# Kernel tuning notes

Measured on AMD Instinct MI355X. Metric: run time of the kernel, lower is better.

The kernel has to match this reference:

```python
import jax, jax.numpy as jnp
import numpy as np

N_NODES = 20000
IN_CH = 512
HEADS = 8
CH = 64  # hidden_layer per head
E = 320000
E_LABEL = 100000


def setup_inputs() -> dict:
    key = jax.random.key(0)
    ks = jax.random.split(key, 8)
    x = jax.random.normal(ks[0], (N_NODES, IN_CH), dtype=jnp.float32)
    edge_index = jax.random.randint(ks[1], (2, E), 0, N_NODES)
    edge_label_index = jax.random.randint(ks[2], (2, E_LABEL), 0, N_NODES)
    # GATv2Conv params (share_weights=False, bias=True)
    sc = 1.0 / np.sqrt(IN_CH)
    W_l = jax.random.normal(ks[3], (IN_CH, HEADS * CH), dtype=jnp.float32) * sc
    W_r = jax.random.normal(ks[4], (IN_CH, HEADS * CH), dtype=jnp.float32) * sc
    att = jax.random.normal(ks[5], (HEADS, CH), dtype=jnp.float32) * (1.0 / np.sqrt(CH))
    bias = jnp.zeros((HEADS * CH,), dtype=jnp.float32)
    gamma = jnp.ones((HEADS * CH,), dtype=jnp.float32)
    beta = jnp.zeros((HEADS * CH,), dtype=jnp.float32)
    return {"x": x, "edge_index": edge_index, "edge_label_index": edge_label_index,
            "W_l": W_l, "W_r": W_r, "att": att, "bias": bias,
            "gamma": gamma, "beta": beta}


def reference(x, edge_index, edge_label_index, W_l, W_r, att, bias, gamma, beta):
    N = x.shape[0]
    H, C = att.shape
    src, dst = edge_index[0], edge_index[1]
    # GATv2Conv: separate source/target linear maps
    xl = (x @ W_l).reshape(N, H, C)
    xr = (x @ W_r).reshape(N, H, C)
    # per-edge attention logits (GATv2: leaky_relu BEFORE attention vector)
    e = jax.nn.leaky_relu(xl[src] + xr[dst], negative_slope=0.2)  # [E,H,C]
    alpha = jnp.einsum('ehc,hc->eh', e, att)                      # [E,H]
    # softmax over incoming edges of each destination node
    amax = jax.ops.segment_max(alpha, dst, num_segments=N)        # [N,H]
    alpha = jnp.exp(alpha - amax[dst])
    denom = jax.ops.segment_sum(alpha, dst, num_segments=N)       # [N,H]
    alpha = alpha / (denom[dst] + 1e-16)
    # scatter-add aggregation of attended source messages
    out = jax.ops.segment_sum(alpha[:, :, None] * xl[src], dst, num_segments=N)  # [N,H,C]
    out = out.reshape(N, H * C) + bias
    # BatchNorm1d (training-mode batch stats, eps=1e-5)
    mu = out.mean(axis=0)
    var = out.var(axis=0)
    out = (out - mu) * jax.lax.rsqrt(var + 1e-5) * gamma + beta
    out = jax.nn.relu(out)  # dropout is identity in deterministic reference
    # gather + dot-product link scoring
    s = out[edge_label_index[0]]
    t = out[edge_label_index[1]]
    return jnp.sum(s * t, axis=1)  # [E_LABEL]
```

## Files before the change

### kernel.cpp

```cpp
#include <hip/hip_runtime.h>
#include <hip/hip_bf16.h>
#include <cstdint>

#define IN_CH 512
#define HC    512
#define HEADS 8
#define NPACK 1024

typedef __attribute__((ext_vector_type(8))) short bf16x8;
typedef __attribute__((ext_vector_type(8))) ushort u16x8;
typedef __attribute__((ext_vector_type(4))) float f32x4;
typedef const __attribute__((address_space(1))) uint8_t* gaddr_t;
typedef __attribute__((address_space(3))) uint8_t* laddr_t;

__device__ inline ushort f2bf(float f) {
  uint32_t u = __float_as_uint(f);
  return (ushort)((u + 0x7fffu + ((u >> 16) & 1u)) >> 16);
}
__device__ inline float bf2f(ushort u) {
  return __uint_as_float(((uint32_t)u) << 16);
}

__global__ void prep(const float* __restrict__ x, ushort* __restrict__ xb,
                     const float* __restrict__ Wl, const float* __restrict__ Wr,
                     ushort* __restrict__ bt,
                     const int* __restrict__ ei, int* __restrict__ counts,
                     const int* __restrict__ eli, int* __restrict__ counts2,
                     int n4, int E, int EL, int nbc, int nbp, int nbh) {
  const int b = blockIdx.x;
  if (b < nbc) {
    const int i = b * 256 + threadIdx.x;
    if (i < n4) {
      const float4 v = ((const float4*)x)[i];
      ushort4 o;
      o.x = f2bf(v.x); o.y = f2bf(v.y); o.z = f2bf(v.z); o.w = f2bf(v.w);
      ((ushort4*)xb)[i] = o;
    }
  } else if (b < nbc + nbp) {
    const int i = (b - nbc) * 256 + threadIdx.x;
    if (i < NPACK * IN_CH) {
      const int n = i >> 9, k = i & 511;
      const float v = (n < HC) ? Wl[(size_t)k * HC + n] : Wr[(size_t)k * HC + (n - HC)];
      bt[i] = f2bf(v);
    }
  } else if (b < nbc + nbp + nbh) {
    const int e = (b - nbc - nbp) * 256 + threadIdx.x;
    if (e < E) atomicAdd(&counts[ei[E + e]], 1);
  } else {
    const int e = (b - nbc - nbp - nbh) * 256 + threadIdx.x;
    if (e < EL) atomicAdd(&counts2[eli[e]], 1);
  }
}

__global__ __launch_bounds__(256) void gemm_mfma(
    const ushort* __restrict__ xb, const ushort* __restrict__ bt,
    ushort* __restrict__ xlb, ushort* __restrict__ xrb, int M) {
  __shared__ __align__(16) ushort As[128 * 32];
  __shared__ __align__(16) ushort Bs[128 * 32];
  const int wave = threadIdx.x >> 6, lane = threadIdx.x & 63;
  const int row0 = blockIdx.y * 128, col0 = blockIdx.x * 128;
  const int quad = lane >> 4, m16 = lane & 15;
  const int wrow = (wave >> 1) * 64, wcol = (wave & 1) * 64;
  const int srow = lane >> 2;
  const int scol = (lane & 3) * 8;
  const f32x4 zero = {0.f, 0.f, 0.f, 0.f};
  f32x4 acc[4][4];
  #pragma unroll
  for (int i = 0; i < 4; ++i)
    #pragma unroll
    for (int j = 0; j < 4; ++j) acc[i][j] = zero;

  for (int k0 = 0; k0 < IN_CH; k0 += 32) {
    #pragma unroll
    for (int c = 0; c < 2; ++c) {
      const int chunk = wave * 2 + c;
      const ushort* ga = xb + (size_t)(row0 + chunk * 16 + srow) * IN_CH + k0 + scol;
      __builtin_amdgcn_global_load_lds((gaddr_t)ga, (laddr_t)(As + chunk * 512), 16, 0, 0);
      const ushort* gb = bt + (size_t)(col0 + chunk * 16 + srow) * IN_CH + k0 + scol;
      __builtin_amdgcn_global_load_lds((gaddr_t)gb, (laddr_t)(Bs + chunk * 512), 16, 0, 0);
    }
    __syncthreads();
    bf16x8 af[4], bfr[4];
    #pragma unroll
    for (int i = 0; i < 4; ++i)
      af[i] = *(const bf16x8*)(As + (wrow + i * 16 + m16) * 32 + quad * 8);
    #pragma unroll
    for (int j = 0; j < 4; ++j)
      bfr[j] = *(const bf16x8*)(Bs + (wcol + j * 16 + m16) * 32 + quad * 8);
    #pragma unroll
    for (int i = 0; i < 4; ++i)
      #pragma unroll
      for (int j = 0; j < 4; ++j)
        acc[i][j] = __builtin_amdgcn_mfma_f32_16x16x32_bf16(af[i], bfr[j], acc[i][j], 0, 0, 0);
    __syncthreads();
  }
  const bool isL = (col0 < HC);
  ushort* dst = isL ? xlb : xrb;
  const int cbase = isL ? col0 : (col0 - HC);
  #pragma unroll
  for (int i = 0; i < 4; ++i) {
    const int r = row0 + wrow + i * 16 + quad * 4;
    #pragma unroll
    for (int j = 0; j < 4; ++j) {
      const int cg = cbase + wcol + j * 16 + m16;
      #pragma unroll
      for (int t = 0; t < 4; ++t) {
        const int rr = r + t;
        if (rr < M) dst[(size_t)rr * HC + cg] = f2bf(acc[i][j][t]);
      }
    }
  }
}

__global__ void scan1(const int* __restrict__ cA, int* __restrict__ oA, int* __restrict__ bA,
                      const int* __restrict__ cB, int* __restrict__ oB, int* __restrict__ bB,
                      int Nn, int nb) {
  const int half = (blockIdx.x >= nb) ? 1 : 0;
  const int blk  = blockIdx.x - half * nb;
  const int* counts = half ? cB : cA;
  int* offsets = half ? oB : oA;
  int* bsums   = half ? bB : bA;
  __shared__ int tmp[256];
  const int t = threadIdx.x;
  const int i = blk * 256 + t;
  const int v = (i < Nn) ? counts[i] : 0;
  tmp[t] = v;
  __syncthreads();
  for (int d = 1; d < 256; d <<= 1) {
    int add = (t >= d) ? tmp[t - d] : 0;
    __syncthreads();
    tmp[t] += add;
    __syncthreads();
  }
  if (i < Nn) offsets[i] = tmp[t] - v;
  if (t == 255) bsums[blk] = tmp[255];
}

__global__ void scan3(int* __restrict__ oA, const int* __restrict__ bA, int* __restrict__ curA,
                      int* __restrict__ oB, const int* __restrict__ bB, int* __restrict__ curB,
                      int Nn, int nb) {
  const int half = (blockIdx.x >= nb) ? 1 : 0;
  const int blk  = blockIdx.x - half * nb;
  int* offsets = half ? oB : oA;
  const int* bsums = half ? bB : bA;
  int* cursor  = half ? curB : curA;
  __shared__ int pref;
  if (threadIdx.x < 64) {
    int s = 0;
    for (int b = threadIdx.x; b < blk; b += 64) s += bsums[b];
    #pragma unroll
    for (int off = 32; off > 0; off >>= 1) s += __shfl_down(s, off, 64);
    if (threadIdx.x == 0) pref = s;
  }
  __syncthreads();
  const int i = blk * 256 + threadIdx.x;
  if (i < Nn) {
    const int o = offsets[i] + pref;
    offsets[i] = o;
    cursor[i] = o;
  }
}

__global__ void csr_fill(const int* __restrict__ ei, int* __restrict__ cursor,
                         int* __restrict__ csr_src,
                         const int* __restrict__ eli, int* __restrict__ cursor2,
                         int* __restrict__ csr_t, int* __restrict__ csr_eid,
                         int E, int EL, int nbE) {
  const int b = blockIdx.x;
  if (b < nbE) {
    const int e = b * 256 + threadIdx.x;
    if (e < E) {
      const int pos = atomicAdd(&cursor[ei[E + e]], 1);
      csr_src[pos] = ei[e];
    }
  } else {
    const int e = (b - nbE) * 256 + threadIdx.x;
    if (e < EL) {
      const int pos = atomicAdd(&cursor2[eli[e]], 1);
      csr_t[pos] = eli[EL + e];
      csr_eid[pos] = e;
    }
  }
}

__global__ __launch_bounds__(256) void gatv2_agg(
    const ushort* __restrict__ xlb, const ushort* xrb, const float* __restrict__ att,
    const int* __restrict__ offsets, const int* __restrict__ counts,
    const int* __restrict__ csr_src, ushort* agg, int Nn) {
  const int node = blockIdx.x * 4 + (threadIdx.x >> 6);
  const int lane = threadIdx.x & 63;
  if (node >= Nn) return;
  const int start = offsets[node];
  const int deg   = counts[node];
  float rv[8], tv[8];
  {
    const u16x8 ur = *(const u16x8*)(xrb + (size_t)node * HC + lane * 8);
    #pragma unroll
    for (int c = 0; c < 8; ++c) rv[c] = bf2f((ushort)ur[c]);
    const float4* pa = (const float4*)(att + lane * 8);
    const float4 t0 = pa[0], t1 = pa[1];
    tv[0]=t0.x; tv[1]=t0.y; tv[2]=t0.z; tv[3]=t0.w;
    tv[4]=t1.x; tv[5]=t1.y; tv[6]=t1.z; tv[7]=t1.w;
  }
  float acc[8] = {};
  float densum = 0.f;
  const int* ps = csr_src + start;
  auto row = [&](int idx) {
    return *(const u16x8*)(xlb + (size_t)ps[idx] * HC + lane * 8);
  };
  auto body = [&](const u16x8 cur) {
    float a[8];
    #pragma unroll
    for (int c = 0; c < 8; ++c) a[c] = bf2f((ushort)cur[c]);
    float s = 0.f;
    #pragma unroll
    for (int c = 0; c < 8; ++c) {
      const float v = a[c] + rv[c];
      s += fmaxf(v, 0.2f * v) * tv[c];
    }
    s += __shfl_xor(s, 1, 8);
    s += __shfl_xor(s, 2, 8);
    s += __shfl_xor(s, 4, 8);
    const float ea = __expf(s);
    densum += ea;
    #pragma unroll
    for (int c = 0; c < 8; ++c) acc[c] += ea * a[c];
  };

  u16x8 b0 = {}, b1 = {}, b2 = {}, b3 = {};
  if (deg > 0) b0 = row(0);
  if (deg > 1) b1 = row(1);
  if (deg > 2) b2 = row(2);
  if (deg > 3) b3 = row(3);
  int i = 0;
  for (; i + 4 <= deg; i += 4) {
    const u16x8 c0 = b0; if (i + 4 < deg) b0 = row(i + 4);
    const u16x8 c1 = b1; if (i + 5 < deg) b1 = row(i + 5);
    const u16x8 c2 = b2; if (i + 6 < deg) b2 = row(i + 6);
    const u16x8 c3 = b3; if (i + 7 < deg) b3 = row(i + 7);
    body(c0); body(c1); body(c2); body(c3);
  }
  const int r = deg - i;
  if (r > 0) body(b0);
  if (r > 1) body(b1);
  if (r > 2) body(b2);

  const float inv = 1.0f / (densum + 1e-16f);
  ushort* pd = agg + (size_t)node * HC + lane * 8;
  ushort4 o0, o1;
  o0.x = f2bf(acc[0] * inv); o0.y = f2bf(acc[1] * inv);
  o0.z = f2bf(acc[2] * inv); o0.w = f2bf(acc[3] * inv);
  o1.x = f2bf(acc[4] * inv); o1.y = f2bf(acc[5] * inv);
  o1.z = f2bf(acc[6] * inv); o1.w = f2bf(acc[7] * inv);
  *(ushort4*)(pd + 0) = o0;
  *(ushort4*)(pd + 4) = o1;
}

__global__ void bn_stats(const ushort* __restrict__ agg, float* __restrict__ gsum,
                         float* __restrict__ gsq, int Nn) {
  const int t = threadIdx.x;
  const int rows_per_block = (Nn + gridDim.x - 1) / gridDim.x;
  const int r0 = blockIdx.x * rows_per_block;
  const int r1 = min(Nn, r0 + rows_per_block);
  float s0 = 0.f, s1 = 0.f, q0 = 0.f, q1 = 0.f;
  for (int r = r0; r < r1; ++r) {
    const ushort2 u = ((const ushort2*)(agg + (size_t)r * HC))[t];
    const float v0 = bf2f(u.x), v1 = bf2f(u.y);
    s0 += v0; q0 += v0 * v0;
    s1 += v1; q1 += v1 * v1;
  }
  atomicAdd(&gsum[2 * t], s0);
  atomicAdd(&gsum[2 * t + 1], s1);
  atomicAdd(&gsq[2 * t], q0);
  atomicAdd(&gsq[2 * t + 1], q1);
}

__global__ void bn_apply(const ushort* __restrict__ agg, const float* __restrict__ gsum,
                         const float* __restrict__ gsq, const float* __restrict__ gamma,
                         const float* __restrict__ beta, ushort* __restrict__ y,
                         float invN, int total4) {
  const int i = blockIdx.x * blockDim.x + threadIdx.x;
  if (i >= total4) return;
  const int base = i << 2;
  const int c = base & (HC - 1);
  const float4 gs = *(const float4*)(gsum + c);
  const float4 gq = *(const float4*)(gsq + c);
  const float4 ga = *(const float4*)(gamma + c);
  const float4 be = *(const float4*)(beta + c);
  const ushort4 u = *(const ushort4*)(agg + base);
  float m, var;
  ushort4 o;
  m = gs.x * invN; var = gq.x * invN - m * m;
  o.x = f2bf(fmaxf(0.f, (bf2f(u.x) - m) * rsqrtf(var + 1e-5f) * ga.x + be.x));
  m = gs.y * invN; var = gq.y * invN - m * m;
  o.y = f2bf(fmaxf(0.f, (bf2f(u.y) - m) * rsqrtf(var + 1e-5f) * ga.y + be.y));
  m = gs.z * invN; var = gq.z * invN - m * m;
  o.z = f2bf(fmaxf(0.f, (bf2f(u.z) - m) * rsqrtf(var + 1e-5f) * ga.z + be.z));
  m = gs.w * invN; var = gq.w * invN - m * m;
  o.w = f2bf(fmaxf(0.f, (bf2f(u.w) - m) * rsqrtf(var + 1e-5f) * ga.w + be.w));
  *(ushort4*)(y + base) = o;
}

__global__ __launch_bounds__(256) void score_g(
    const ushort* __restrict__ y, const int* __restrict__ off2,
    const int* __restrict__ cnt2, const int* __restrict__ csr_t,
    const int* __restrict__ csr_eid, float* __restrict__ out, int Nn) {
  const int node = blockIdx.x * 4 + (threadIdx.x >> 6);
  const int lane = threadIdx.x & 63;
  if (node >= Nn) return;
  const int start = off2[node];
  const int deg   = cnt2[node];
  if (deg == 0) return;
  float a[8];
  {
    const u16x8 us = *(const u16x8*)(y + (size_t)node * HC + lane * 8);
    #pragma unroll
    for (int c = 0; c < 8; ++c) a[c] = bf2f((ushort)us[c]);
  }
  const int* pt = csr_t + start;
  const int* pe = csr_eid + start;
  auto row = [&](int idx) {
    return *(const u16x8*)(y + (size_t)pt[idx] * HC + lane * 8);
  };
  auto emit = [&](const u16x8 ut, int eid) {
    float s = 0.f;
    #pragma unroll
    for (int c = 0; c < 8; ++c) s += a[c] * bf2f((ushort)ut[c]);
    #pragma unroll
    for (int off = 32; off > 0; off >>= 1) s += __shfl_down(s, off, 64);
    if (lane == 0) out[eid] = s;
  };
  u16x8 b0 = {}, b1 = {}, b2 = {}, b3 = {};
  b0 = row(0);
  if (deg > 1) b1 = row(1);
  if (deg > 2) b2 = row(2);
  if (deg > 3) b3 = row(3);
  int j = 0;
  for (; j + 4 <= deg; j += 4) {
    const u16x8 c0 = b0; if (j + 4 < deg) b0 = row(j + 4);
    const u16x8 c1 = b1; if (j + 5 < deg) b1 = row(j + 5);
    const u16x8 c2 = b2; if (j + 6 < deg) b2 = row(j + 6);
    const u16x8 c3 = b3; if (j + 7 < deg) b3 = row(j + 7);
    emit(c0, pe[j]); emit(c1, pe[j + 1]); emit(c2, pe[j + 2]); emit(c3, pe[j + 3]);
  }
  const int r = deg - j;
  if (r > 0) emit(b0, pe[j]);
  if (r > 1) emit(b1, pe[j + 1]);
  if (r > 2) emit(b2, pe[j + 2]);
}

extern "C" void kernel_launch(void* const* d_in, const int* in_sizes, int n_in,
                              void* d_out, int out_size, void* d_ws, size_t ws_size,
                              hipStream_t stream) {
  const float* x     = (const float*)d_in[0];
  const int*   ei    = (const int*)d_in[1];
  const int*   eli   = (const int*)d_in[2];
  const float* W_l   = (const float*)d_in[3];
  const float* W_r   = (const float*)d_in[4];
  const float* att   = (const float*)d_in[5];
  const float* gamma = (const float*)d_in[7];
  const float* beta  = (const float*)d_in[8];
  float* out = (float*)d_out;

  const int Nn = in_sizes[0] / IN_CH;
  const int E  = in_sizes[1] / 2;
  const int EL = in_sizes[2] / 2;

  ushort* xlb = (ushort*)d_ws;
  ushort* xrb = xlb + (size_t)Nn * HC;
  ushort* xbf = xrb + (size_t)Nn * HC;
  ushort* btb = xbf + (size_t)Nn * IN_CH;
  int* counts   = (int*)(btb + (size_t)NPACK * IN_CH);
  int* counts2  = counts + Nn;
  float* gsum   = (float*)(counts2 + Nn);
  float* gsq    = gsum + HC;
  int* offsets  = (int*)(gsq + HC);
  int* cursor   = offsets + Nn;
  int* bsumsA   = cursor + Nn;
  int* offsets2 = bsumsA + 256;
  int* cursor2  = offsets2 + Nn;
  int* bsumsB   = cursor2 + Nn;
  int* csr_src  = bsumsB + 256;
  int* csr_t    = csr_src + E;
  int* csr_eid  = csr_t + EL;
  ushort* agg = xrb;
  ushort* y   = xlb;

  const int nb  = (Nn + 255) / 256;
  const int nbc = (Nn * IN_CH / 4 + 255) / 256;
  const int nbp = (NPACK * IN_CH + 255) / 256;
  const int nbh = (E + 255) / 256;
  const int nbh2 = (EL + 255) / 256;

  hipMemsetAsync(counts, 0, (2 * (size_t)Nn + 2 * HC) * sizeof(int), stream);

  prep<<<nbc + nbp + nbh + nbh2, 256, 0, stream>>>(
      x, xbf, W_l, W_r, btb, ei, counts, eli, counts2,
      Nn * IN_CH / 4, E, EL, nbc, nbp, nbh);

  dim3 ggrid(NPACK / 128, (Nn + 127) / 128);
  gemm_mfma<<<ggrid, 256, 0, stream>>>(xbf, btb, xlb, xrb, Nn);

  scan1<<<2 * nb, 256, 0, stream>>>(counts, offsets, bsumsA,
                                    counts2, offsets2, bsumsB, Nn, nb);
  scan3<<<2 * nb, 256, 0, stream>>>(offsets, bsumsA, cursor,
                                    offsets2, bsumsB, cursor2, Nn, nb);
  csr_fill<<<nbh + nbh2, 256, 0, stream>>>(ei, cursor, csr_src,
                                           eli, cursor2, csr_t, csr_eid, E, EL, nbh);

  gatv2_agg<<<(Nn + 3) / 4, 256, 0, stream>>>(xlb, xrb, att, offsets, counts,
                                              csr_src, agg, Nn);

  bn_stats<<<200, 256, 0, stream>>>(agg, gsum, gsq, Nn);
  bn_apply<<<(Nn * HC / 4 + 255) / 256, 256, 0, stream>>>(
      agg, gsum, gsq, gamma, beta, y, 1.0f / (float)Nn, Nn * HC / 4);

  score_g<<<(Nn + 3) / 4, 256, 0, stream>>>(y, offsets2, counts2, csr_t, csr_eid,
                                            out, Nn);
}
```

Baseline: 318.6 us.

## Split GATv2 aggregation across two waves per node and shrink prefetch depth

The aggregation kernel now assigns two wavefronts per destination node, each handling half of the 512 channels with 4 elements per lane. The per-head reduction uses a 16-lane shuffle instead of an 8-lane one. Both the aggregation and scoring kernels cut their gather prefetch depth from 4 rows to 2. This doubles the number of independent waves available to hide gather latency, at the cost of narrower loads, reloading the index list and xr row in both halves, and less per-wave memory-level parallelism.

```diff
diff --git a/kernel.cpp b/kernel.cpp
--- a/kernel.cpp
+++ b/kernel.cpp
@@ -187,73 +187,65 @@
     const ushort* __restrict__ xlb, const ushort* xrb, const float* __restrict__ att,
     const int* __restrict__ offsets, const int* __restrict__ counts,
     const int* __restrict__ csr_src, ushort* agg, int Nn) {
-  const int node = blockIdx.x * 4 + (threadIdx.x >> 6);
+  const int wid  = blockIdx.x * 4 + (threadIdx.x >> 6);
+  const int node = wid >> 1;
+  const int half = wid & 1;
   const int lane = threadIdx.x & 63;
   if (node >= Nn) return;
+  const int cb = half * 256 + lane * 4;
   const int start = offsets[node];
   const int deg   = counts[node];
-  float rv[8], tv[8];
+  float rv[4], tv[4];
   {
-    const u16x8 ur = *(const u16x8*)(xrb + (size_t)node * HC + lane * 8);
-    #pragma unroll
-    for (int c = 0; c < 8; ++c) rv[c] = bf2f((ushort)ur[c]);
-    const float4* pa = (const float4*)(att + lane * 8);
-    const float4 t0 = pa[0], t1 = pa[1];
-    tv[0]=t0.x; tv[1]=t0.y; tv[2]=t0.z; tv[3]=t0.w;
-    tv[4]=t1.x; tv[5]=t1.y; tv[6]=t1.z; tv[7]=t1.w;
-  }
-  float acc[8] = {};
+    const ushort4 ur = *(const ushort4*)(xrb + (size_t)node * HC + cb);
+    rv[0] = bf2f(ur.x); rv[1] = bf2f(ur.y); rv[2] = bf2f(ur.z); rv[3] = bf2f(ur.w);
+    const float4 t = *(const float4*)(att + cb);
+    tv[0] = t.x; tv[1] = t.y; tv[2] = t.z; tv[3] = t.w;
+  }
+  float acc[4] = {};
   float densum = 0.f;
   const int* ps = csr_src + start;
   auto row = [&](int idx) {
-    return *(const u16x8*)(xlb + (size_t)ps[idx] * HC + lane * 8);
+    return *(const ushort4*)(xlb + (size_t)ps[idx] * HC + cb);
   };
-  auto body = [&](const u16x8 cur) {
-    float a[8];
-    #pragma unroll
-    for (int c = 0; c < 8; ++c) a[c] = bf2f((ushort)cur[c]);
+  auto body = [&](const ushort4 cur) {
+    float a[4];
+    a[0] = bf2f(cur.x); a[1] = bf2f(cur.y); a[2] = bf2f(cur.z); a[3] = bf2f(cur.w);
     float s = 0.f;
     #pragma unroll
-    for (int c = 0; c < 8; ++c) {
+    for (int c = 0; c < 4; ++c) {
       const float v = a[c] + rv[c];
       s += fmaxf(v, 0.2f * v) * tv[c];
     }
-    s += __shfl_xor(s, 1, 8);
-    s += __shfl_xor(s, 2, 8);
-    s += __shfl_xor(s, 4, 8);
+    s += __shfl_xor(s, 1, 16);
+    s += __shfl_xor(s, 2, 16);
+    s += __shfl_xor(s, 4, 16);
+    s += __shfl_xor(s, 8, 16);
     const float ea = __expf(s);
     densum += ea;
     #pragma unroll
-    for (int c = 0; c < 8; ++c) acc[c] += ea * a[c];
+    for (int c = 0; c < 4; ++c) acc[c] += ea * a[c];
   };
 
-  u16x8 b0 = {}, b1 = {}, b2 = {}, b3 = {};
+  ushort4 b0 = {0, 0, 0, 0}, b1 = {0, 0, 0, 0};
   if (deg > 0) b0 = row(0);
   if (deg > 1) b1 = row(1);
-  if (deg > 2) b2 = row(2);
-  if (deg > 3) b3 = row(3);
   int i = 0;
-  for (; i + 4 <= deg; i += 4) {
-    const u16x8 c0 = b0; if (i + 4 < deg) b0 = row(i + 4);
-    const u16x8 c1 = b1; if (i + 5 < deg) b1 = row(i + 5);
-    const u16x8 c2 = b2; if (i + 6 < deg) b2 = row(i + 6);
-    const u16x8 c3 = b3; if (i + 7 < deg) b3 = row(i + 7);
-    body(c0); body(c1); body(c2); body(c3);
-  }
-  const int r = deg - i;
-  if (r > 0) body(b0);
-  if (r > 1) body(b1);
-  if (r > 2) body(b2);
+  for (; i + 2 <= deg; i += 2) {
+    const ushort4 c0 = b0;
+    if (i + 2 < deg) b0 = row(i + 2);
+    const ushort4 c1 = b1;
+    if (i + 3 < deg) b1 = row(i + 3);
+    body(c0);
+    body(c1);
+  }
+  if (i < deg) body(b0);
 
   const float inv = 1.0f / (densum + 1e-16f);
-  ushort* pd = agg + (size_t)node * HC + lane * 8;
-  ushort4 o0, o1;
-  o0.x = f2bf(acc[0] * inv); o0.y = f2bf(acc[1] * inv);
-  o0.z = f2bf(acc[2] * inv); o0.w = f2bf(acc[3] * inv);
-  o1.x = f2bf(acc[4] * inv); o1.y = f2bf(acc[5] * inv);
-  o1.z = f2bf(acc[6] * inv); o1.w = f2bf(acc[7] * inv);
-  *(ushort4*)(pd + 0) = o0;
-  *(ushort4*)(pd + 4) = o1;
+  ushort4 o;
+  o.x = f2bf(acc[0] * inv); o.y = f2bf(acc[1] * inv);
+  o.z = f2bf(acc[2] * inv); o.w = f2bf(acc[3] * inv);
+  *(ushort4*)(agg + (size_t)node * HC + cb) = o;
 }
 
 __global__ void bn_stats(const ushort* __restrict__ agg, float* __restrict__ gsum,
@@ -330,23 +322,19 @@
     for (int off = 32; off > 0; off >>= 1) s += __shfl_down(s, off, 64);
     if (lane == 0) out[eid] = s;
   };
-  u16x8 b0 = {}, b1 = {}, b2 = {}, b3 = {};
+  u16x8 b0 = {}, b1 = {};
   b0 = row(0);
   if (deg > 1) b1 = row(1);
-  if (deg > 2) b2 = row(2);
-  if (deg > 3) b3 = row(3);
   int j = 0;
-  for (; j + 4 <= deg; j += 4) {
-    const u16x8 c0 = b0; if (j + 4 < deg) b0 = row(j + 4);
-    const u16x8 c1 = b1; if (j + 5 < deg) b1 = row(j + 5);
-    const u16x8 c2 = b2; if (j + 6 < deg) b2 = row(j + 6);
-    const u16x8 c3 = b3; if (j + 7 < deg) b3 = row(j + 7);
-    emit(c0, pe[j]); emit(c1, pe[j + 1]); emit(c2, pe[j + 2]); emit(c3, pe[j + 3]);
-  }
-  const int r = deg - j;
-  if (r > 0) emit(b0, pe[j]);
-  if (r > 1) emit(b1, pe[j + 1]);
-  if (r > 2) emit(b2, pe[j + 2]);
+  for (; j + 2 <= deg; j += 2) {
+    const u16x8 c0 = b0;
+    if (j + 2 < deg) b0 = row(j + 2);
+    const u16x8 c1 = b1;
+    if (j + 3 < deg) b1 = row(j + 3);
+    emit(c0, pe[j]);
+    emit(c1, pe[j + 1]);
+  }
+  if (j < deg) emit(b0, pe[j]);
 }
 
 extern "C" void kernel_launch(void* const* d_in, const int* in_sizes, int n_in,
@@ -408,8 +396,8 @@
   csr_fill<<<nbh + nbh2, 256, 0, stream>>>(ei, cursor, csr_src,
                                            eli, cursor2, csr_t, csr_eid, E, EL, nbh);
 
-  gatv2_agg<<<(Nn + 3) / 4, 256, 0, stream>>>(xlb, xrb, att, offsets, counts,
-                                              csr_src, agg, Nn);
+  gatv2_agg<<<(2 * Nn + 3) / 4, 256, 0, stream>>>(xlb, xrb, att, offsets, counts,
+                                                  csr_src, agg, Nn);
 
   bn_stats<<<200, 256, 0, stream>>>(agg, gsum, gsq, Nn);
   bn_apply<<<(Nn * HC / 4 + 255) / 256, 256, 0, stream>>>(
```

After: 317.2 us. About the same (-0.5%).
